# Performance work log

Hardware: AMD Instinct MI355X
Metric: run time of the kernel (lower is better)

The kernel has to match this reference:

```python
import jax, jax.numpy as jnp
import numpy as np

# StyleLossDiag: diag(gram(x)) vs precomputed target diag, MSE loss.
# diag(F @ F.T) == sum(F**2, axis=1), so we never materialize the
# (a*b)x(a*b) Gram matrix -- same math, O(n) instead of O(n^2 d).

A, B, C, D = 16, 512, 64, 64  # target_feature_shape


def gram_diag(x):
    a, b, c, d = x.shape
    feats = x.reshape(a * b, c * d)
    # diagonal of (feats @ feats.T) / (a*b*c*d)
    return jnp.sum(feats * feats, axis=1) / (a * b * c * d)


def setup_inputs() -> dict:
    key = jax.random.key(0)
    k1, k2 = jax.random.split(key)
    x = jax.random.normal(k1, (A, B, C, D), dtype=jnp.float32)
    # target buffer: diag(gram(target_feature)).detach() from __init__
    target_feature = jax.random.normal(k2, (A, B, C, D), dtype=jnp.float32)
    target = gram_diag(target_feature)  # shape [A*B] = [8192]
    return {"x": x, "target": target}


def reference(x, target):
    g = gram_diag(x)                      # [a*b]
    loss = jnp.mean((g - target) ** 2)    # F.mse_loss default 'mean'
    return loss
```

## Files before the change

kernel.cpp:

```cpp
#include <hip/hip_runtime.h>


#define ROWS   8192
#define ROWLEN 4096
#define INV_NORM (1.0f / 33554432.0f)

__global__ __launch_bounds__(256) void rowdiag_kernel(
    const float* __restrict__ x,
    const float* __restrict__ target,
    float* __restrict__ ws)
{
    const int row = blockIdx.x;
    const float4* xr = reinterpret_cast<const float4*>(x) + (size_t)row * (ROWLEN / 4);

    float s = 0.0f;
#pragma unroll
    for (int i = 0; i < 4; ++i) {
        float4 v = xr[threadIdx.x + i * 256];
        s += v.x * v.x + v.y * v.y + v.z * v.z + v.w * v.w;
    }

#pragma unroll
    for (int off = 32; off > 0; off >>= 1)
        s += __shfl_down(s, off, 64);

    __shared__ float lds[4];
    const int lane = threadIdx.x & 63;
    const int wave = threadIdx.x >> 6;
    if (lane == 0) lds[wave] = s;
    __syncthreads();

    if (threadIdx.x == 0) {
        float tot = (lds[0] + lds[1]) + (lds[2] + lds[3]);
        float d = tot * INV_NORM - target[row];
        ws[row] = d * d;
    }
}

__global__ __launch_bounds__(256) void final_reduce_kernel(
    const float* __restrict__ ws,
    float* __restrict__ out)
{
    float s = 0.0f;
#pragma unroll
    for (int i = 0; i < ROWS / 256; ++i)
        s += ws[threadIdx.x + i * 256];

#pragma unroll
    for (int off = 32; off > 0; off >>= 1)
        s += __shfl_down(s, off, 64);

    __shared__ float lds[4];
    const int lane = threadIdx.x & 63;
    const int wave = threadIdx.x >> 6;
    if (lane == 0) lds[wave] = s;
    __syncthreads();

    if (threadIdx.x == 0)
        out[0] = ((lds[0] + lds[1]) + (lds[2] + lds[3])) * (1.0f / (float)ROWS);
}

extern "C" void kernel_launch(void* const* d_in, const int* in_sizes, int n_in,
                              void* d_out, int out_size, void* d_ws, size_t ws_size,
                              hipStream_t stream)
{
    const float* x      = (const float*)d_in[0];
    const float* target = (const float*)d_in[1];
    float* out = (float*)d_out;
    float* ws  = (float*)d_ws;

    rowdiag_kernel<<<ROWS, 256, 0, stream>>>(x, target, ws);
    final_reduce_kernel<<<1, 256, 0, stream>>>(ws, out);
}
```

Before: 26.86 us.

## Assign one wavefront per row and vectorize final reduction loads

The row-reduction kernel now gives each 64-lane wavefront a whole 4096-element row, with four rows per 256-thread block. This removes the LDS write and __syncthreads, and cuts the block count by four. Each lane issues 16 float4 loads into four independent accumulators to raise memory-level parallelism. The final reduce reads the workspace as float4. The change also alters the floating-point summation order.

```diff
diff --git a/kernel.cpp b/kernel.cpp
--- a/kernel.cpp
+++ b/kernel.cpp
@@ -1,38 +1,41 @@
 #include <hip/hip_runtime.h>
 
 
-#define ROWS   8192
-#define ROWLEN 4096
+#define ROWS     8192
+#define ROWLEN   4096
 #define INV_NORM (1.0f / 33554432.0f)
 
-__global__ __launch_bounds__(256) void rowdiag_kernel(
+__global__ __launch_bounds__(256) void rowdiag_wave_kernel(
     const float* __restrict__ x,
     const float* __restrict__ target,
     float* __restrict__ ws)
 {
-    const int row = blockIdx.x;
+    const int wave = threadIdx.x >> 6;
+    const int lane = threadIdx.x & 63;
+    const int row  = blockIdx.x * 4 + wave;
+
     const float4* xr = reinterpret_cast<const float4*>(x) + (size_t)row * (ROWLEN / 4);
 
-    float s = 0.0f;
+    float a0 = 0.f, a1 = 0.f, a2 = 0.f, a3 = 0.f;
 #pragma unroll
     for (int i = 0; i < 4; ++i) {
-        float4 v = xr[threadIdx.x + i * 256];
-        s += v.x * v.x + v.y * v.y + v.z * v.z + v.w * v.w;
+        float4 v0 = xr[lane + (4 * i + 0) * 64];
+        float4 v1 = xr[lane + (4 * i + 1) * 64];
+        float4 v2 = xr[lane + (4 * i + 2) * 64];
+        float4 v3 = xr[lane + (4 * i + 3) * 64];
+        a0 += v0.x * v0.x + v0.y * v0.y + v0.z * v0.z + v0.w * v0.w;
+        a1 += v1.x * v1.x + v1.y * v1.y + v1.z * v1.z + v1.w * v1.w;
+        a2 += v2.x * v2.x + v2.y * v2.y + v2.z * v2.z + v2.w * v2.w;
+        a3 += v3.x * v3.x + v3.y * v3.y + v3.z * v3.z + v3.w * v3.w;
     }
+    float s = (a0 + a1) + (a2 + a3);
 
 #pragma unroll
     for (int off = 32; off > 0; off >>= 1)
         s += __shfl_down(s, off, 64);
 
-    __shared__ float lds[4];
-    const int lane = threadIdx.x & 63;
-    const int wave = threadIdx.x >> 6;
-    if (lane == 0) lds[wave] = s;
-    __syncthreads();
-
-    if (threadIdx.x == 0) {
-        float tot = (lds[0] + lds[1]) + (lds[2] + lds[3]);
-        float d = tot * INV_NORM - target[row];
+    if (lane == 0) {
+        float d = s * INV_NORM - target[row];
         ws[row] = d * d;
     }
 }
@@ -41,10 +44,13 @@
     const float* __restrict__ ws,
     float* __restrict__ out)
 {
-    float s = 0.0f;
+    const float4* w4 = reinterpret_cast<const float4*>(ws);
+    float s = 0.f;
 #pragma unroll
-    for (int i = 0; i < ROWS / 256; ++i)
-        s += ws[threadIdx.x + i * 256];
+    for (int i = 0; i < ROWS / 4 / 256; ++i) {
+        float4 v = w4[threadIdx.x + i * 256];
+        s += (v.x + v.y) + (v.z + v.w);
+    }
 
 #pragma unroll
     for (int off = 32; off > 0; off >>= 1)
@@ -69,6 +75,6 @@
     float* out = (float*)d_out;
     float* ws  = (float*)d_ws;
 
-    rowdiag_kernel<<<ROWS, 256, 0, stream>>>(x, target, ws);
+    rowdiag_wave_kernel<<<ROWS / 4, 256, 0, stream>>>(x, target, ws);
     final_reduce_kernel<<<1, 256, 0, stream>>>(ws, out);
 }
```

Result: no change. 26.90 us (+0.2%).
